# Kernel tuning notes

Measured on AMD Instinct MI355X. Metric: run time of the kernel, lower is better.

## Reference

```python
import jax, jax.numpy as jnp
import numpy as np

B, S, D_IN, D_OUT, H = 2, 2048, 1024, 1024, 16
HD = D_OUT // H


def setup_inputs() -> dict:
    key = jax.random.key(0)
    ks = jax.random.split(key, 6)
    x = jax.random.normal(ks[0], (B, S, D_IN), jnp.float32)
    Wq = jax.random.normal(ks[1], (D_IN, D_OUT), jnp.float32) * 0.02
    Wk = jax.random.normal(ks[2], (D_IN, D_OUT), jnp.float32) * 0.02
    Wv = jax.random.normal(ks[3], (D_IN, D_OUT), jnp.float32) * 0.02
    Wo = jax.random.normal(ks[4], (D_OUT, D_OUT), jnp.float32) * 0.02
    bo = jax.random.normal(ks[5], (D_OUT,), jnp.float32) * 0.02
    return {"x": x, "Wq": Wq, "Wk": Wk, "Wv": Wv, "Wo": Wo, "bo": bo}


def reference(x, Wq, Wk, Wv, Wo, bo):
    b, s, _ = x.shape

    def to_heads(t):  # [b, s, d_out] -> [b, h, s, hd]
        return t.reshape(b, s, H, HD).transpose(0, 2, 1, 3)

    Q = to_heads(x @ Wq)
    K = to_heads(x @ Wk)
    V = to_heads(x @ Wv)

    scale = 1.0 / jnp.sqrt(jnp.asarray(HD, x.dtype))
    scores = jnp.einsum("bhqd,bhkd->bhqk", Q, K) * scale
    causal_mask = jnp.triu(jnp.ones((s, s), dtype=bool), k=1)  # True above diag
    scores = jnp.where(causal_mask, jnp.asarray(-1e6, scores.dtype), scores)
    weights = jax.nn.softmax(scores, axis=-1)  # dropout p=0.0 -> identity
    attn = jnp.einsum("bhqk,bhkd->bhqd", weights, V)  # [b, h, s, hd]
    # Faithful to source: reshape [b,h,s,hd] -> [b,s,d_out] WITHOUT head transpose-back
    attn = attn.reshape(b, s, D_OUT)
    return attn @ Wo + bo
```

## Files before the change

kernel.cpp:

```cpp
#include <hip/hip_runtime.h>
#include <stdint.h>


typedef unsigned short u16;
typedef __attribute__((ext_vector_type(8))) short bf16x8;
typedef __attribute__((ext_vector_type(4))) float f32x4;

#define MFMA_BF16(a, b, c) __builtin_amdgcn_mfma_f32_16x16x32_bf16((a), (b), (c), 0, 0, 0)
#define QSCALE 0.18033688011112042f

__device__ __forceinline__ u16 f2bf(float f) {
  union { float f; unsigned int u; } x; x.f = f;
  unsigned int r = x.u + 0x7fffu + ((x.u >> 16) & 1u);
  return (u16)(r >> 16);
}
__device__ __forceinline__ bf16x8 pack8(float4 a, float4 b) {
  bf16x8 r;
  r[0] = (short)f2bf(a.x); r[1] = (short)f2bf(a.y);
  r[2] = (short)f2bf(a.z); r[3] = (short)f2bf(a.w);
  r[4] = (short)f2bf(b.x); r[5] = (short)f2bf(b.y);
  r[6] = (short)f2bf(b.z); r[7] = (short)f2bf(b.w);
  return r;
}
__device__ __forceinline__ void gload_lds16(const u16* g, u16* l) {
  __builtin_amdgcn_global_load_lds((__attribute__((address_space(1))) void*)g,
                                   (__attribute__((address_space(3))) void*)l, 16, 0, 0);
}

template <int CPR>
__device__ __forceinline__ int sw_off(int r, int c) {
  return (r * CPR + (c ^ (r & (CPR - 1)))) * 8;
}

__global__ __launch_bounds__(256) void x_to_bf16(const float* __restrict__ x,
                                                 u16* __restrict__ xb) {
  const size_t i = ((size_t)blockIdx.x * 256 + threadIdx.x) * 8;
  const float4 a = *(const float4*)&x[i];
  const float4 b = *(const float4*)&x[i + 4];
  *(bf16x8*)&xb[i] = pack8(a, b);
}

__global__ void transpose_cols(const float* __restrict__ W0, const float* __restrict__ W1,
                               const float* __restrict__ W2, u16* __restrict__ T,
                               int h0, int hsx64) {
  __shared__ u16 t[32][33];
  const int j0 = blockIdx.x * 32;
  const int g = j0 / hsx64;
  const float* W = (g == 0) ? W0 : (g == 1) ? W1 : W2;
  const int wc0 = h0 * 64 + (j0 % hsx64);
  const int k0 = blockIdx.y * 32;
  t[threadIdx.y][threadIdx.x] =
      f2bf(W[(size_t)(k0 + threadIdx.y) * 1024 + wc0 + threadIdx.x]);
  __syncthreads();
  T[(size_t)(j0 + threadIdx.y) * 1024 + k0 + threadIdx.x] = t[threadIdx.x][threadIdx.y];
}

template <int MODE, int AF32>
__global__ __launch_bounds__(256, 2) void gemm_bt(
    const void* __restrict__ Av, const u16* __restrict__ BT,
    void* __restrict__ C0v, u16* __restrict__ C1, u16* __restrict__ C2,
    const float* __restrict__ bias, int M, int N, int K, int hs, int h0) {
  __shared__ __align__(16) u16 lsA[128 * 32];
  __shared__ __align__(16) u16 lsB[128 * 32];
  const int tid = threadIdx.x, lane = tid & 63, wv = tid >> 6;
  const int quad = lane >> 4, l16 = lane & 15;
  const int m0 = blockIdx.y * 128, n0 = blockIdx.x * 128;
  const int wm = (wv >> 1) * 64, wn = (wv & 1) * 64;
  const int hs64 = hs * 64;
  f32x4 acc[4][4] = {};

  for (int k0 = 0; k0 < K; k0 += 32) {
    if constexpr (AF32) {
      bf16x8 va[2], vb[2];
#pragma unroll
      for (int c = 0; c < 2; ++c) {
        const int P = c * 256 + tid, r = P >> 2, cc = P & 3;
        const float* Af = (const float*)Av;
        const float4 a0 = *(const float4*)&Af[(size_t)(m0 + r) * K + k0 + cc * 8];
        const float4 a1 = *(const float4*)&Af[(size_t)(m0 + r) * K + k0 + cc * 8 + 4];
        va[c] = pack8(a0, a1);
        vb[c] = *(const bf16x8*)&BT[(size_t)(n0 + r) * K + k0 + cc * 8];
      }
      __syncthreads();
#pragma unroll
      for (int c = 0; c < 2; ++c) {
        const int P = c * 256 + tid, r = P >> 2, cc = P & 3;
        *(bf16x8*)&lsA[sw_off<4>(r, cc)] = va[c];
        *(bf16x8*)&lsB[sw_off<4>(r, cc)] = vb[c];
      }
      __syncthreads();
    } else {
      __syncthreads();
#pragma unroll
      for (int c = 0; c < 2; ++c) {
        const int P = c * 256 + tid, r = P >> 2;
        const int gcol = ((P & 3) ^ (r & 3)) * 8;
        gload_lds16((const u16*)Av + (size_t)(m0 + r) * K + k0 + gcol,
                    &lsA[(size_t)(c * 256 + wv * 64) * 8]);
        gload_lds16(BT + (size_t)(n0 + r) * K + k0 + gcol,
                    &lsB[(size_t)(c * 256 + wv * 64) * 8]);
      }
      __syncthreads();
    }
    bf16x8 af[4], bfr[4];
#pragma unroll
    for (int i = 0; i < 4; ++i) af[i] = *(const bf16x8*)&lsA[sw_off<4>(wm + i * 16 + l16, quad)];
#pragma unroll
    for (int j = 0; j < 4; ++j) bfr[j] = *(const bf16x8*)&lsB[sw_off<4>(wn + j * 16 + l16, quad)];
#pragma unroll
    for (int i = 0; i < 4; ++i)
#pragma unroll
      for (int j = 0; j < 4; ++j) acc[i][j] = MFMA_BF16(af[i], bfr[j], acc[i][j]);
  }

#pragma unroll
  for (int i = 0; i < 4; ++i)
#pragma unroll
    for (int j = 0; j < 4; ++j) {
      const int n = n0 + wn + j * 16 + l16;
      float bv = 0.f;
      if constexpr (MODE == 1) bv = bias[n];
#pragma unroll
      for (int r = 0; r < 4; ++r) {
        const int m = m0 + wm + i * 16 + quad * 4 + r;
        if constexpr (MODE == 3) {
          const int b = m >> 11, s = m & 2047;
          if (n < hs64) {
            ((u16*)C0v)[((size_t)b * 2048 + s) * hs64 + n] = f2bf(acc[i][j][r] * QSCALE);
          } else if (n < 2 * hs64) {
            C1[((size_t)b * 2048 + s) * hs64 + (n - hs64)] = f2bf(acc[i][j][r]);
          } else {
            const int nn = n - 2 * hs64;
            C2[((size_t)(b * hs + (nn >> 6)) * 64 + (nn & 63)) * 2048 + s] =
                f2bf(acc[i][j][r]);
          }
        } else {
          const int b = (m >= hs * 128) ? 1 : 0;
          const int rp = m - b * hs * 128;
          ((float*)C0v)[(size_t)(b * 2048 + h0 * 128 + rp) * 1024 + n] =
              acc[i][j][r] + bv;
        }
      }
    }
}

__global__ __launch_bounds__(256, 4) void attn_fwd(
    const u16* __restrict__ Qsl, const u16* __restrict__ Ksl,
    const u16* __restrict__ VTsl, u16* __restrict__ A2sl, int hs) {
  __shared__ __align__(16) u16 lsK[2][64 * 64];
  __shared__ __align__(16) u16 lsV[2][64 * 64];
  __shared__ __align__(16) u16 lsP[4][16 * 64];
  const int tid = threadIdx.x, lane = tid & 63, wv = tid >> 6;
  const int quad = lane >> 4, l16 = lane & 15;

  const int cpx = gridDim.x >> 3;
  const int w = (blockIdx.x & 7) * cpx + (blockIdx.x >> 3);
  const int bh = w >> 4;
  const int bx = w & 15;

  const int b = (bh >= hs) ? 1 : 0, hh = bh - b * hs;
  const int hs64 = hs * 64;
  const int wm = wv * 16;
  const u16* Qb = Qsl + (size_t)b * 2048 * hs64;
  const u16* Kb = Ksl + (size_t)b * 2048 * hs64;
  const u16* Vb = VTsl + (size_t)(b * hs + hh) * 64 * 2048;
  u16* A2b = A2sl + (size_t)(b * hs + hh) * 2048 * 64;
  u16* lsPw = &lsP[wv][0];

  bf16x8 ones;
#pragma unroll
  for (int i = 0; i < 8; ++i) ones[i] = (short)0x3F80;

  for (int half = 0; half < 2; ++half) {
    const int qt = (half == 0) ? bx : 31 - bx;
    const int q0 = qt * 64;

    bf16x8 qf[2];
#pragma unroll
    for (int ks = 0; ks < 2; ++ks)
      qf[ks] = *(const bf16x8*)&Qb[(size_t)(q0 + wm + l16) * hs64 + hh * 64 +
                                   ks * 32 + quad * 8];

    f32x4 acc_o[4] = {};
    f32x4 acc_l = {};

    __syncthreads();
#pragma unroll
    for (int c = 0; c < 2; ++c) {
      const int P = c * 256 + tid;
      const int r = P >> 3, cc = (P & 7) ^ (r & 7);
      gload_lds16(Kb + (size_t)r * hs64 + hh * 64 + cc * 8,
                  &lsK[0][(c * 256 + wv * 64) * 8]);
      gload_lds16(Vb + (size_t)r * 2048 + cc * 8,
                  &lsV[0][(c * 256 + wv * 64) * 8]);
    }

    for (int kt = 0; kt <= qt; ++kt) {
      const int k0 = kt * 64;
      const int buf = kt & 1;
      __syncthreads();
      if (kt < qt) {
        const int k1 = k0 + 64;
        const int nb = buf ^ 1;
#pragma unroll
        for (int c = 0; c < 2; ++c) {
          const int P = c * 256 + tid;
          const int r = P >> 3, cc = (P & 7) ^ (r & 7);
          gload_lds16(Kb + (size_t)(k1 + r) * hs64 + hh * 64 + cc * 8,
                      &lsK[nb][(c * 256 + wv * 64) * 8]);
          gload_lds16(Vb + (size_t)r * 2048 + k1 + cc * 8,
                      &lsV[nb][(c * 256 + wv * 64) * 8]);
        }
      }

      f32x4 accs[4] = {};
#pragma unroll
      for (int ks = 0; ks < 2; ++ks)
#pragma unroll
        for (int nj = 0; nj < 4; ++nj) {
          const bf16x8 kf =
              *(const bf16x8*)&lsK[buf][sw_off<8>(nj * 16 + l16, ks * 4 + quad)];
          accs[nj] = MFMA_BF16(kf, qf[ks], accs[nj]);
        }

      const bool diag = (kt == qt);
      const int grow = q0 + wm + l16;
#pragma unroll
      for (int ks2 = 0; ks2 < 2; ++ks2) {
#pragma unroll
        for (int njh = 0; njh < 2; ++njh) {
          const int nj = ks2 * 2 + njh;
          const int keyb = k0 + nj * 16 + quad * 4;
#pragma unroll
          for (int r = 0; r < 4; ++r) {
            float p = exp2f(accs[nj][r]);
            if (diag) p = (keyb + r > grow) ? 0.f : p;
            accs[nj][r] = p;
          }
          union { float f; unsigned int u; } t0, t1, t2, t3;
          t0.f = accs[nj][0]; t1.f = accs[nj][1];
          t2.f = accs[nj][2]; t3.f = accs[nj][3];
          uint2 wpk;
          wpk.x = (t0.u >> 16) | (t1.u & 0xFFFF0000u);
          wpk.y = (t2.u >> 16) | (t3.u & 0xFFFF0000u);
          const int idx = (l16 * 64 + nj * 16 + quad * 4) ^ ((l16 & 7) << 3);
          *(uint2*)&lsPw[idx] = wpk;
        }
        const int pidx = (l16 * 64 + ks2 * 32 + quad * 8) ^ ((l16 & 7) << 3);
        const bf16x8 pf = *(const bf16x8*)&lsPw[pidx];
        acc_l = MFMA_BF16(ones, pf, acc_l);
#pragma unroll
        for (int njo = 0; njo < 4; ++njo) {
          const bf16x8 vf =
              *(const bf16x8*)&lsV[buf][sw_off<8>(njo * 16 + l16, ks2 * 4 + quad)];
          acc_o[njo] = MFMA_BF16(vf, pf, acc_o[njo]);
        }
      }
    }

    const float inv = 1.0f / acc_l[0];
#pragma unroll
    for (int njo = 0; njo < 4; ++njo) {
      uint2 o;
      o.x = (unsigned)f2bf(acc_o[njo][0] * inv) |
            ((unsigned)f2bf(acc_o[njo][1] * inv) << 16);
      o.y = (unsigned)f2bf(acc_o[njo][2] * inv) |
            ((unsigned)f2bf(acc_o[njo][3] * inv) << 16);
      *(uint2*)&A2b[(size_t)(q0 + wm + l16) * 64 + njo * 16 + quad * 4] = o;
    }
  }
}

extern "C" void kernel_launch(void* const* d_in, const int* in_sizes, int n_in,
                              void* d_out, int out_size, void* d_ws, size_t ws_size,
                              hipStream_t stream) {
  (void)in_sizes; (void)n_in; (void)out_size;
  const float* x  = (const float*)d_in[0];
  const float* Wq = (const float*)d_in[1];
  const float* Wk = (const float*)d_in[2];
  const float* Wv = (const float*)d_in[3];
  const float* Wo = (const float*)d_in[4];
  const float* bo = (const float*)d_in[5];
  float* out = (float*)d_out;
  char* ws = (char*)d_ws;
  const size_t MB = 1024 * 1024;
  const size_t KB = 1024;

  int hs = 2;
  if      (ws_size >= 2 * MB + 16 * 2432 * KB) hs = 16;
  else if (ws_size >= 2 * MB +  8 * 2432 * KB) hs = 8;
  else if (ws_size >= 2 * MB +  4 * 2432 * KB) hs = 4;

  u16* WoT   = (u16*)(ws);
  u16* Ksl   = (u16*)(ws + 2 * MB);
  u16* VTsl  = (u16*)(ws + 2 * MB + (size_t)hs *  512 * KB);
  u16* A2sl  = (u16*)(ws + 2 * MB + (size_t)hs * 1024 * KB);
  u16* WT3sl = (u16*)(ws + 2 * MB + (size_t)hs * 1536 * KB);
  u16* Qsl   = (u16*)(ws + 2 * MB + (size_t)hs * 1920 * KB);

  transpose_cols<<<dim3(32, 32), dim3(32, 32), 0, stream>>>(Wo, Wo, Wo, WoT, 0, 1024);
  if (hs == 16) {
    u16* xb = A2sl;
    x_to_bf16<<<2048, 256, 0, stream>>>(x, xb);
    transpose_cols<<<dim3(96, 32), dim3(32, 32), 0, stream>>>(Wq, Wk, Wv, WT3sl, 0, 1024);
    gemm_bt<3, 0><<<dim3(24, 32), 256, 0, stream>>>(
        (const void*)xb, WT3sl, (void*)Qsl, Ksl, VTsl, nullptr, 4096, 3072, 1024, 16, 0);
    attn_fwd<<<dim3(512), 256, 0, stream>>>(Qsl, Ksl, VTsl, A2sl, 16);
    gemm_bt<1, 0><<<dim3(8, 32), 256, 0, stream>>>(
        (const void*)A2sl, WoT, (void*)out, nullptr, nullptr, bo, 4096, 1024, 1024, 16, 0);
  } else {
    for (int h0 = 0; h0 < 16; h0 += hs) {
      transpose_cols<<<dim3(6 * hs, 32), dim3(32, 32), 0, stream>>>(Wq, Wk, Wv, WT3sl, h0, hs * 64);
      gemm_bt<3, 1><<<dim3((3 * hs) / 2, 32), 256, 0, stream>>>(
          (const void*)x, WT3sl, (void*)Qsl, Ksl, VTsl, nullptr, 4096, 3 * hs * 64, 1024, hs, h0);
      attn_fwd<<<dim3(16 * 2 * hs), 256, 0, stream>>>(Qsl, Ksl, VTsl, A2sl, hs);
      gemm_bt<1, 0><<<dim3(8, 2 * hs), 256, 0, stream>>>(
          (const void*)A2sl, WoT, (void*)out, nullptr, nullptr, bo, 2 * hs * 128, 1024, 1024, hs, h0);
    }
  }
}
```

Baseline: 199.4 us.

## Split attention key tiles across two wave groups with LDS reduction

Doubles the attention block to 512 threads. Each of two 4-wave groups handles half of every 64-key tile (32 keys), so per-wave QK and PV work is halved and there are more waves in flight. Group 1 writes its partial output and row sums to LDS, reusing the K buffer, and group 0 combines them, normalizes and stores. This adds an extra reduction phase with two barriers and raises thread count per block, which may limit occupancy under launch_bounds(512,4).

```diff
diff --git a/kernel.cpp b/kernel.cpp
--- a/kernel.cpp
+++ b/kernel.cpp
@@ -144,14 +144,18 @@
     }
 }
 
-__global__ __launch_bounds__(256, 4) void attn_fwd(
+__global__ __launch_bounds__(512, 4) void attn_fwd(
     const u16* __restrict__ Qsl, const u16* __restrict__ Ksl,
     const u16* __restrict__ VTsl, u16* __restrict__ A2sl, int hs) {
   __shared__ __align__(16) u16 lsK[2][64 * 64];
   __shared__ __align__(16) u16 lsV[2][64 * 64];
-  __shared__ __align__(16) u16 lsP[4][16 * 64];
+  __shared__ __align__(16) u16 lsP[8][16 * 32];
+  __shared__ __align__(16) float scrl[64];
   const int tid = threadIdx.x, lane = tid & 63, wv = tid >> 6;
   const int quad = lane >> 4, l16 = lane & 15;
+  const int grp = wv >> 2;
+  const int wq = wv & 3;
+  const int wm = wq * 16;
 
   const int cpx = gridDim.x >> 3;
   const int w = (blockIdx.x & 7) * cpx + (blockIdx.x >> 3);
@@ -160,12 +164,12 @@
 
   const int b = (bh >= hs) ? 1 : 0, hh = bh - b * hs;
   const int hs64 = hs * 64;
-  const int wm = wv * 16;
   const u16* Qb = Qsl + (size_t)b * 2048 * hs64;
   const u16* Kb = Ksl + (size_t)b * 2048 * hs64;
   const u16* Vb = VTsl + (size_t)(b * hs + hh) * 64 * 2048;
   u16* A2b = A2sl + (size_t)(b * hs + hh) * 2048 * 64;
   u16* lsPw = &lsP[wv][0];
+  float* scro = (float*)&lsK[0][0];
 
   bf16x8 ones;
 #pragma unroll
@@ -185,14 +189,10 @@
     f32x4 acc_l = {};
 
     __syncthreads();
-#pragma unroll
-    for (int c = 0; c < 2; ++c) {
-      const int P = c * 256 + tid;
-      const int r = P >> 3, cc = (P & 7) ^ (r & 7);
-      gload_lds16(Kb + (size_t)r * hs64 + hh * 64 + cc * 8,
-                  &lsK[0][(c * 256 + wv * 64) * 8]);
-      gload_lds16(Vb + (size_t)r * 2048 + cc * 8,
-                  &lsV[0][(c * 256 + wv * 64) * 8]);
+    {
+      const int r = tid >> 3, cc = (tid & 7) ^ (r & 7);
+      gload_lds16(Kb + (size_t)r * hs64 + hh * 64 + cc * 8, &lsK[0][wv * 512]);
+      gload_lds16(Vb + (size_t)r * 2048 + cc * 8, &lsV[0][wv * 512]);
     }
 
     for (int kt = 0; kt <= qt; ++kt) {
@@ -200,73 +200,79 @@
       const int buf = kt & 1;
       __syncthreads();
       if (kt < qt) {
-        const int k1 = k0 + 64;
-        const int nb = buf ^ 1;
-#pragma unroll
-        for (int c = 0; c < 2; ++c) {
-          const int P = c * 256 + tid;
-          const int r = P >> 3, cc = (P & 7) ^ (r & 7);
-          gload_lds16(Kb + (size_t)(k1 + r) * hs64 + hh * 64 + cc * 8,
-                      &lsK[nb][(c * 256 + wv * 64) * 8]);
-          gload_lds16(Vb + (size_t)r * 2048 + k1 + cc * 8,
-                      &lsV[nb][(c * 256 + wv * 64) * 8]);
-        }
-      }
-
-      f32x4 accs[4] = {};
+        const int k1 = k0 + 64, nb = buf ^ 1;
+        const int r = tid >> 3, cc = (tid & 7) ^ (r & 7);
+        gload_lds16(Kb + (size_t)(k1 + r) * hs64 + hh * 64 + cc * 8,
+                    &lsK[nb][wv * 512]);
+        gload_lds16(Vb + (size_t)r * 2048 + k1 + cc * 8, &lsV[nb][wv * 512]);
+      }
+
+      f32x4 accs[2] = {};
 #pragma unroll
       for (int ks = 0; ks < 2; ++ks)
 #pragma unroll
-        for (int nj = 0; nj < 4; ++nj) {
-          const bf16x8 kf =
-              *(const bf16x8*)&lsK[buf][sw_off<8>(nj * 16 + l16, ks * 4 + quad)];
+        for (int nj = 0; nj < 2; ++nj) {
+          const bf16x8 kf = *(const bf16x8*)
+              &lsK[buf][sw_off<8>(grp * 32 + nj * 16 + l16, ks * 4 + quad)];
           accs[nj] = MFMA_BF16(kf, qf[ks], accs[nj]);
         }
 
       const bool diag = (kt == qt);
       const int grow = q0 + wm + l16;
 #pragma unroll
-      for (int ks2 = 0; ks2 < 2; ++ks2) {
-#pragma unroll
-        for (int njh = 0; njh < 2; ++njh) {
-          const int nj = ks2 * 2 + njh;
-          const int keyb = k0 + nj * 16 + quad * 4;
-#pragma unroll
-          for (int r = 0; r < 4; ++r) {
-            float p = exp2f(accs[nj][r]);
-            if (diag) p = (keyb + r > grow) ? 0.f : p;
-            accs[nj][r] = p;
-          }
-          union { float f; unsigned int u; } t0, t1, t2, t3;
-          t0.f = accs[nj][0]; t1.f = accs[nj][1];
-          t2.f = accs[nj][2]; t3.f = accs[nj][3];
-          uint2 wpk;
-          wpk.x = (t0.u >> 16) | (t1.u & 0xFFFF0000u);
-          wpk.y = (t2.u >> 16) | (t3.u & 0xFFFF0000u);
-          const int idx = (l16 * 64 + nj * 16 + quad * 4) ^ ((l16 & 7) << 3);
-          *(uint2*)&lsPw[idx] = wpk;
+      for (int nj = 0; nj < 2; ++nj) {
+        const int keyb = k0 + grp * 32 + nj * 16 + quad * 4;
+#pragma unroll
+        for (int r = 0; r < 4; ++r) {
+          float p = exp2f(accs[nj][r]);
+          if (diag) p = (keyb + r > grow) ? 0.f : p;
+          accs[nj][r] = p;
         }
-        const int pidx = (l16 * 64 + ks2 * 32 + quad * 8) ^ ((l16 & 7) << 3);
-        const bf16x8 pf = *(const bf16x8*)&lsPw[pidx];
-        acc_l = MFMA_BF16(ones, pf, acc_l);
-#pragma unroll
-        for (int njo = 0; njo < 4; ++njo) {
-          const bf16x8 vf =
-              *(const bf16x8*)&lsV[buf][sw_off<8>(njo * 16 + l16, ks2 * 4 + quad)];
-          acc_o[njo] = MFMA_BF16(vf, pf, acc_o[njo]);
-        }
-      }
-    }
-
-    const float inv = 1.0f / acc_l[0];
-#pragma unroll
-    for (int njo = 0; njo < 4; ++njo) {
-      uint2 o;
-      o.x = (unsigned)f2bf(acc_o[njo][0] * inv) |
-            ((unsigned)f2bf(acc_o[njo][1] * inv) << 16);
-      o.y = (unsigned)f2bf(acc_o[njo][2] * inv) |
-            ((unsigned)f2bf(acc_o[njo][3] * inv) << 16);
-      *(uint2*)&A2b[(size_t)(q0 + wm + l16) * 64 + njo * 16 + quad * 4] = o;
+        union { float f; unsigned int u; } t0, t1, t2, t3;
+        t0.f = accs[nj][0]; t1.f = accs[nj][1];
+        t2.f = accs[nj][2]; t3.f = accs[nj][3];
+        uint2 wpk;
+        wpk.x = (t0.u >> 16) | (t1.u & 0xFFFF0000u);
+        wpk.y = (t2.u >> 16) | (t3.u & 0xFFFF0000u);
+        const int idx =
+            l16 * 32 + (((nj * 4 + quad) ^ ((l16 & 3) << 1)) << 2);
+        *(uint2*)&lsPw[idx] = wpk;
+      }
+
+      const int pidx = l16 * 32 + ((quad ^ (l16 & 3)) << 3);
+      const bf16x8 pf = *(const bf16x8*)&lsPw[pidx];
+      acc_l = MFMA_BF16(ones, pf, acc_l);
+#pragma unroll
+      for (int njo = 0; njo < 4; ++njo) {
+        const bf16x8 vf = *(const bf16x8*)
+            &lsV[buf][sw_off<8>(njo * 16 + l16, grp * 4 + quad)];
+        acc_o[njo] = MFMA_BF16(vf, pf, acc_o[njo]);
+      }
+    }
+
+    __syncthreads();
+    if (grp == 1) {
+#pragma unroll
+      for (int njo = 0; njo < 4; ++njo) {
+        const int ch = (njo * 4 + quad) ^ l16;
+        *(f32x4*)&scro[(size_t)(wm + l16) * 64 + ch * 4] = acc_o[njo];
+      }
+      if (quad == 0) scrl[wm + l16] = acc_l[0];
+    }
+    __syncthreads();
+    if (grp == 0) {
+      const float inv = 1.0f / (acc_l[0] + scrl[wm + l16]);
+#pragma unroll
+      for (int njo = 0; njo < 4; ++njo) {
+        const int ch = (njo * 4 + quad) ^ l16;
+        const f32x4 ob = *(const f32x4*)&scro[(size_t)(wm + l16) * 64 + ch * 4];
+        uint2 o;
+        o.x = (unsigned)f2bf((acc_o[njo][0] + ob[0]) * inv) |
+              ((unsigned)f2bf((acc_o[njo][1] + ob[1]) * inv) << 16);
+        o.y = (unsigned)f2bf((acc_o[njo][2] + ob[2]) * inv) |
+              ((unsigned)f2bf((acc_o[njo][3] + ob[3]) * inv) << 16);
+        *(uint2*)&A2b[(size_t)(q0 + wm + l16) * 64 + njo * 16 + quad * 4] = o;
+      }
     }
   }
 }
@@ -305,7 +311,7 @@
     transpose_cols<<<dim3(96, 32), dim3(32, 32), 0, stream>>>(Wq, Wk, Wv, WT3sl, 0, 1024);
     gemm_bt<3, 0><<<dim3(24, 32), 256, 0, stream>>>(
         (const void*)xb, WT3sl, (void*)Qsl, Ksl, VTsl, nullptr, 4096, 3072, 1024, 16, 0);
-    attn_fwd<<<dim3(512), 256, 0, stream>>>(Qsl, Ksl, VTsl, A2sl, 16);
+    attn_fwd<<<dim3(512), 512, 0, stream>>>(Qsl, Ksl, VTsl, A2sl, 16);
     gemm_bt<1, 0><<<dim3(8, 32), 256, 0, stream>>>(
         (const void*)A2sl, WoT, (void*)out, nullptr, nullptr, bo, 4096, 1024, 1024, 16, 0);
   } else {
@@ -313,7 +319,7 @@
       transpose_cols<<<dim3(6 * hs, 32), dim3(32, 32), 0, stream>>>(Wq, Wk, Wv, WT3sl, h0, hs * 64);
       gemm_bt<3, 1><<<dim3((3 * hs) / 2, 32), 256, 0, stream>>>(
           (const void*)x, WT3sl, (void*)Qsl, Ksl, VTsl, nullptr, 4096, 3 * hs * 64, 1024, hs, h0);
-      attn_fwd<<<dim3(16 * 2 * hs), 256, 0, stream>>>(Qsl, Ksl, VTsl, A2sl, hs);
+      attn_fwd<<<dim3(32 * hs), 512, 0, stream>>>(Qsl, Ksl, VTsl, A2sl, hs);
       gemm_bt<1, 0><<<dim3(8, 2 * hs), 256, 0, stream>>>(
           (const void*)A2sl, WoT, (void*)out, nullptr, nullptr, bo, 2 * hs * 128, 1024, 1024, hs, h0);
     }
```

Result: no change. 199.8 us (+0.2%).

## Split attention key tile across wave pairs with 32-row query tiles and LDS reduction

Applied to the files above, without the earlier changes.

Each wave now processes 32 query rows against half of the 64-key tile, instead of 16 query rows against the full tile. Each K and V fragment read from LDS therefore feeds two MFMAs, which halves LDS fragment traffic per MFMA. The two key-half partial outputs and row sums are combined through an LDS scratch area (reusing the K buffer) before normalisation and the bf16 store. In exchange, register pressure rises (launch bounds relaxed from 4 to 2 blocks per SM, which may cut occupancy), and each query tile gains an extra reduction with two barriers.

```diff
diff --git a/kernel.cpp b/kernel.cpp
--- a/kernel.cpp
+++ b/kernel.cpp
@@ -144,14 +144,17 @@
     }
 }
 
-__global__ __launch_bounds__(256, 4) void attn_fwd(
+__global__ __launch_bounds__(256, 2) void attn_fwd(
     const u16* __restrict__ Qsl, const u16* __restrict__ Ksl,
     const u16* __restrict__ VTsl, u16* __restrict__ A2sl, int hs) {
   __shared__ __align__(16) u16 lsK[2][64 * 64];
   __shared__ __align__(16) u16 lsV[2][64 * 64];
   __shared__ __align__(16) u16 lsP[4][16 * 64];
+  __shared__ __align__(16) float scrl[64];
   const int tid = threadIdx.x, lane = tid & 63, wv = tid >> 6;
   const int quad = lane >> 4, l16 = lane & 15;
+  const int grp = wv >> 1;
+  const int wq = wv & 1;
 
   const int cpx = gridDim.x >> 3;
   const int w = (blockIdx.x & 7) * cpx + (blockIdx.x >> 3);
@@ -160,29 +163,34 @@
 
   const int b = (bh >= hs) ? 1 : 0, hh = bh - b * hs;
   const int hs64 = hs * 64;
-  const int wm = wv * 16;
   const u16* Qb = Qsl + (size_t)b * 2048 * hs64;
   const u16* Kb = Ksl + (size_t)b * 2048 * hs64;
   const u16* Vb = VTsl + (size_t)(b * hs + hh) * 64 * 2048;
   u16* A2b = A2sl + (size_t)(b * hs + hh) * 2048 * 64;
   u16* lsPw = &lsP[wv][0];
+  float* scro = (float*)&lsK[0][0];
 
   bf16x8 ones;
 #pragma unroll
   for (int i = 0; i < 8; ++i) ones[i] = (short)0x3F80;
+
+  const int prow = l16 >> 1;
+  const int pb0 = (l16 & 1) << 2;
 
   for (int half = 0; half < 2; ++half) {
     const int qt = (half == 0) ? bx : 31 - bx;
     const int q0 = qt * 64;
 
-    bf16x8 qf[2];
-#pragma unroll
-    for (int ks = 0; ks < 2; ++ks)
-      qf[ks] = *(const bf16x8*)&Qb[(size_t)(q0 + wm + l16) * hs64 + hh * 64 +
-                                   ks * 32 + quad * 8];
-
-    f32x4 acc_o[4] = {};
-    f32x4 acc_l = {};
+    bf16x8 qf[2][2];
+#pragma unroll
+    for (int j = 0; j < 2; ++j)
+#pragma unroll
+      for (int ks = 0; ks < 2; ++ks)
+        qf[j][ks] = *(const bf16x8*)&Qb[(size_t)(q0 + wq * 32 + j * 16 + l16) * hs64 +
+                                        hh * 64 + ks * 32 + quad * 8];
+
+    f32x4 acc_o[2][4] = {};
+    f32x4 acc_l[2] = {};
 
     __syncthreads();
 #pragma unroll
@@ -191,8 +199,7 @@
       const int r = P >> 3, cc = (P & 7) ^ (r & 7);
       gload_lds16(Kb + (size_t)r * hs64 + hh * 64 + cc * 8,
                   &lsK[0][(c * 256 + wv * 64) * 8]);
-      gload_lds16(Vb + (size_t)r * 2048 + cc * 8,
-                  &lsV[0][(c * 256 + wv * 64) * 8]);
+      gload_lds16(Vb + (size_t)r * 2048 + cc * 8, &lsV[0][(c * 256 + wv * 64) * 8]);
     }
 
     for (int kt = 0; kt <= qt; ++kt) {
@@ -200,8 +207,7 @@
       const int buf = kt & 1;
       __syncthreads();
       if (kt < qt) {
-        const int k1 = k0 + 64;
-        const int nb = buf ^ 1;
+        const int k1 = k0 + 64, nb = buf ^ 1;
 #pragma unroll
         for (int c = 0; c < 2; ++c) {
           const int P = c * 256 + tid;
@@ -213,60 +219,90 @@
         }
       }
 
-      f32x4 accs[4] = {};
+      f32x4 accs[2][2] = {};
 #pragma unroll
       for (int ks = 0; ks < 2; ++ks)
 #pragma unroll
-        for (int nj = 0; nj < 4; ++nj) {
-          const bf16x8 kf =
-              *(const bf16x8*)&lsK[buf][sw_off<8>(nj * 16 + l16, ks * 4 + quad)];
-          accs[nj] = MFMA_BF16(kf, qf[ks], accs[nj]);
+        for (int nj = 0; nj < 2; ++nj) {
+          const bf16x8 kf = *(const bf16x8*)
+              &lsK[buf][sw_off<8>(grp * 32 + nj * 16 + l16, ks * 4 + quad)];
+          accs[0][nj] = MFMA_BF16(kf, qf[0][ks], accs[0][nj]);
+          accs[1][nj] = MFMA_BF16(kf, qf[1][ks], accs[1][nj]);
         }
 
       const bool diag = (kt == qt);
-      const int grow = q0 + wm + l16;
-#pragma unroll
-      for (int ks2 = 0; ks2 < 2; ++ks2) {
-#pragma unroll
-        for (int njh = 0; njh < 2; ++njh) {
-          const int nj = ks2 * 2 + njh;
-          const int keyb = k0 + nj * 16 + quad * 4;
+#pragma unroll
+      for (int j = 0; j < 2; ++j) {
+        const int grow = q0 + wq * 32 + j * 16 + l16;
+#pragma unroll
+        for (int nj = 0; nj < 2; ++nj) {
+          const int keyb = k0 + grp * 32 + nj * 16 + quad * 4;
 #pragma unroll
           for (int r = 0; r < 4; ++r) {
-            float p = exp2f(accs[nj][r]);
+            float p = exp2f(accs[j][nj][r]);
             if (diag) p = (keyb + r > grow) ? 0.f : p;
-            accs[nj][r] = p;
+            accs[j][nj][r] = p;
           }
           union { float f; unsigned int u; } t0, t1, t2, t3;
-          t0.f = accs[nj][0]; t1.f = accs[nj][1];
-          t2.f = accs[nj][2]; t3.f = accs[nj][3];
+          t0.f = accs[j][nj][0]; t1.f = accs[j][nj][1];
+          t2.f = accs[j][nj][2]; t3.f = accs[j][nj][3];
           uint2 wpk;
           wpk.x = (t0.u >> 16) | (t1.u & 0xFFFF0000u);
           wpk.y = (t2.u >> 16) | (t3.u & 0xFFFF0000u);
-          const int idx = (l16 * 64 + nj * 16 + quad * 4) ^ ((l16 & 7) << 3);
-          *(uint2*)&lsPw[idx] = wpk;
-        }
-        const int pidx = (l16 * 64 + ks2 * 32 + quad * 8) ^ ((l16 & 7) << 3);
-        const bf16x8 pf = *(const bf16x8*)&lsPw[pidx];
-        acc_l = MFMA_BF16(ones, pf, acc_l);
+          const int row = j * 8 + prow;
+          const int chunk = (pb0 + 2 * nj + (quad >> 1)) ^ prow;
+          *(uint2*)&lsPw[row * 64 + chunk * 8 + (quad & 1) * 4] = wpk;
+        }
+      }
+
+      bf16x8 pf[2];
+#pragma unroll
+      for (int j = 0; j < 2; ++j) {
+        const int row = j * 8 + prow;
+        const int chunk = (pb0 + quad) ^ prow;
+        pf[j] = *(const bf16x8*)&lsPw[row * 64 + chunk * 8];
+        acc_l[j] = MFMA_BF16(ones, pf[j], acc_l[j]);
+      }
+#pragma unroll
+      for (int njo = 0; njo < 4; ++njo) {
+        const bf16x8 vf = *(const bf16x8*)
+            &lsV[buf][sw_off<8>(njo * 16 + l16, grp * 4 + quad)];
+        acc_o[0][njo] = MFMA_BF16(vf, pf[0], acc_o[0][njo]);
+        acc_o[1][njo] = MFMA_BF16(vf, pf[1], acc_o[1][njo]);
+      }
+    }
+
+    __syncthreads();
+    if (grp == 1) {
+#pragma unroll
+      for (int j = 0; j < 2; ++j) {
 #pragma unroll
         for (int njo = 0; njo < 4; ++njo) {
-          const bf16x8 vf =
-              *(const bf16x8*)&lsV[buf][sw_off<8>(njo * 16 + l16, ks2 * 4 + quad)];
-          acc_o[njo] = MFMA_BF16(vf, pf, acc_o[njo]);
-        }
-      }
-    }
-
-    const float inv = 1.0f / acc_l[0];
-#pragma unroll
-    for (int njo = 0; njo < 4; ++njo) {
-      uint2 o;
-      o.x = (unsigned)f2bf(acc_o[njo][0] * inv) |
-            ((unsigned)f2bf(acc_o[njo][1] * inv) << 16);
-      o.y = (unsigned)f2bf(acc_o[njo][2] * inv) |
-            ((unsigned)f2bf(acc_o[njo][3] * inv) << 16);
-      *(uint2*)&A2b[(size_t)(q0 + wm + l16) * 64 + njo * 16 + quad * 4] = o;
+          const int ch = (njo * 4 + quad) ^ l16;
+          *(f32x4*)&scro[(size_t)(wq * 32 + j * 16 + l16) * 64 + ch * 4] =
+              acc_o[j][njo];
+        }
+        if (quad == 0) scrl[wq * 32 + j * 16 + l16] = acc_l[j][0];
+      }
+    }
+    __syncthreads();
+    if (grp == 0) {
+#pragma unroll
+      for (int j = 0; j < 2; ++j) {
+        const int ql = wq * 32 + j * 16 + l16;
+        const float inv = 1.0f / (acc_l[j][0] + scrl[ql]);
+#pragma unroll
+        for (int njo = 0; njo < 4; ++njo) {
+          const int ch = (njo * 4 + quad) ^ l16;
+          const f32x4 ob = *(const f32x4*)&scro[(size_t)ql * 64 + ch * 4];
+          uint2 o;
+          o.x = (unsigned)f2bf((acc_o[j][njo][0] + ob[0]) * inv) |
+                ((unsigned)f2bf((acc_o[j][njo][1] + ob[1]) * inv) << 16);
+          o.y = (unsigned)f2bf((acc_o[j][njo][2] + ob[2]) * inv) |
+                ((unsigned)f2bf((acc_o[j][njo][3] + ob[3]) * inv) << 16);
+          *(uint2*)&A2b[(size_t)(q0 + ql) * 64 + njo * 16 + quad * 4] = o;
+        }
+      }
     }
   }
 }
```

Result: no change. 198.2 us (-0.6%).
